# Kernel optimization log

Measured on AMD Instinct MI355X. Metric: run time of the kernel, lower is better.

Reference implementation:

```python
import jax, jax.numpy as jnp
import numpy as np

L, H = 6, 8          # depth, heads
DM, DH, M = 512, 64, 256  # d_model, d_head, nb random features
EPS = 1e-4


def sinusoidal_pe(n, d, dtype):
    pos = jnp.arange(n, dtype=jnp.float32)[:, None]
    div = jnp.exp(jnp.arange(0, d, 2, dtype=jnp.float32) * (-(np.log(10000.0) / d)))
    pe = jnp.zeros((n, d), jnp.float32)
    pe = pe.at[:, 0::2].set(jnp.sin(pos * div))
    pe = pe.at[:, 1::2].set(jnp.cos(pos * div))
    return pe.astype(dtype)


def layer_norm(x, g, b, eps=1e-5):
    mu = jnp.mean(x, -1, keepdims=True)
    var = jnp.mean(jnp.square(x - mu), -1, keepdims=True)
    return (x - mu) * jax.lax.rsqrt(var + eps) * g + b


def softmax_features(x, proj, is_query):
    # FAVOR+ positive softmax-kernel features. x: [b,h,n,dh], proj: [m,dh]
    dn = DH ** -0.25
    xd = x * dn
    u = jnp.einsum('bhnd,md->bhnm', xd, proj)            # [b,h,n,m]
    diag = 0.5 * jnp.sum(xd * xd, -1, keepdims=True)      # ||x||^2/2 (normalized)
    if is_query:
        stab = jnp.max(u, axis=-1, keepdims=True)
    else:
        stab = jnp.max(u, axis=(-2, -1), keepdims=True)
    return (M ** -0.5) * (jnp.exp(u - diag - stab) + EPS)


def split_heads(t, b, n):
    return t.reshape(b, n, H, DH).transpose(0, 2, 1, 3)   # [b,h,n,dh]


def reference(x, proj, ln1_g, ln1_b, wq, wk, wv, wo, bo, ln2_g, ln2_b, w1, b1, w2, b2):
    b, n, d = x.shape
    x = x + sinusoidal_pe(n, d, x.dtype)[None]
    for i in range(L):
        # --- FAVOR+ linear attention (pre-norm) ---
        h = layer_norm(x, ln1_g[i], ln1_b[i])
        q = split_heads(h @ wq[i], b, n)
        k = split_heads(h @ wk[i], b, n)
        v = split_heads(h @ wv[i], b, n)
        qp = softmax_features(q, proj[i], True)           # [b,h,n,m]
        kp = softmax_features(k, proj[i], False)
        ksum = jnp.sum(kp, axis=2)                         # [b,h,m]
        d_inv = 1.0 / jnp.einsum('bhnm,bhm->bhn', qp, ksum)
        ctx = jnp.einsum('bhnm,bhnd->bhmd', kp, v)         # [b,h,m,dh]
        o = jnp.einsum('bhnm,bhmd->bhnd', qp, ctx) * d_inv[..., None]
        o = o.transpose(0, 2, 1, 3).reshape(b, n, DM)
        x = x + o @ wo[i] + bo[i]
        # --- feed-forward (pre-norm, GELU) ---
        h = layer_norm(x, ln2_g[i], ln2_b[i])
        x = x + jax.nn.gelu(h @ w1[i] + b1[i], approximate=False) @ w2[i] + b2[i]
    return x


def setup_inputs() -> dict:
    key = jax.random.key(0)
    ks = jax.random.split(key, 9)
    s_in = DM ** -0.5
    s_ff = (4 * DM) ** -0.5
    return {
        'x':     jax.random.normal(ks[0], (8, 2048, DM), jnp.float32),
        'proj':  jax.random.normal(ks[1], (L, M, DH), jnp.float32),
        'ln1_g': jnp.ones((L, DM), jnp.float32),
        'ln1_b': jnp.zeros((L, DM), jnp.float32),
        'wq':    jax.random.normal(ks[2], (L, DM, DM), jnp.float32) * s_in,
        'wk':    jax.random.normal(ks[3], (L, DM, DM), jnp.float32) * s_in,
        'wv':    jax.random.normal(ks[4], (L, DM, DM), jnp.float32) * s_in,
        'wo':    jax.random.normal(ks[5], (L, DM, DM), jnp.float32) * s_in,
        'bo':    jnp.zeros((L, DM), jnp.float32),
        'ln2_g': jnp.ones((L, DM), jnp.float32),
        'ln2_b': jnp.zeros((L, DM), jnp.float32),
        'w1':    jax.random.normal(ks[6], (L, DM, 4 * DM), jnp.float32) * s_in,
        'b1':    jnp.zeros((L, 4 * DM), jnp.float32),
        'w2':    jax.random.normal(ks[7], (L, 4 * DM, DM), jnp.float32) * s_ff,
        'b2':    jnp.zeros((L, DM), jnp.float32),
    }
```

## Files before the change

kernel.cpp:

```cpp
#include <hip/hip_runtime.h>
#include <math.h>

#define LNUM 6
#define HNUM 8
#define DMODEL 512
#define DHEAD 64
#define MFEAT 256
#define BATCH 8
#define SEQ 2048
#define TOK (BATCH*SEQ)
#define BHN (BATCH*HNUM)
#define DFF 2048
#define EPSF 1e-4f
#define LN_EPS 1e-5f
#define DNRM 0.35355339059327373f
#define SMF 0.0625f

typedef unsigned short u16;
typedef __attribute__((ext_vector_type(8))) short bf16x8;
typedef __attribute__((ext_vector_type(4))) float f32x4;
#define MFMA16(a,b,c) __builtin_amdgcn_mfma_f32_16x16x32_bf16(a,b,c,0,0,0)

#define GLOAD16(g,l) __builtin_amdgcn_global_load_lds( \
    (const __attribute__((address_space(1))) void*)(g), \
    (__attribute__((address_space(3))) void*)(l), 16, 0, 0)

__device__ __forceinline__ u16 f2bf(float f){
  unsigned int u = __float_as_uint(f);
  u = (u + 0x7fffu + ((u >> 16) & 1u)) >> 16;
  return (u16)u;
}
__device__ __forceinline__ float bf2f(u16 s){
  return __uint_as_float(((unsigned int)s) << 16);
}
__device__ __forceinline__ void atomicMaxF(float* addr, float val){
  if(val >= 0.f) atomicMax((int*)addr, __float_as_int(val));
  else           atomicMin((unsigned int*)addr, __float_as_uint(val));
}
__device__ __forceinline__ float fast_gelu(float z){
  float g2 = z*(1.5957691216f + 0.07135481628f*z*z);
  return z / (1.0f + __expf(-g2));
}

__global__ void k_addpe(const float* __restrict__ x, float* __restrict__ xo){
  int idx = blockIdx.x*256 + threadIdx.x;
  int d = idx & (DMODEL-1);
  int n = (idx >> 9) & (SEQ-1);
  int j = d >> 1;
  float freq = expf((float)(2*j) * (-9.210340371976184f / (float)DMODEL));
  float ang = (float)n * freq;
  float pe = (d & 1) ? cosf(ang) : sinf(ang);
  xo[idx] = x[idx] + pe;
}

__global__ void k_ln(const float* __restrict__ x, const float* __restrict__ g,
                     const float* __restrict__ bv, u16* __restrict__ out){
  __shared__ float sred[8];
  int t = blockIdx.x, tid = threadIdx.x;
  const float2 v = ((const float2*)(x + (size_t)t*DMODEL))[tid];
  float s = v.x + v.y;
  #pragma unroll
  for(int o=32;o;o>>=1) s += __shfl_down(s,o);
  if((tid&63)==0) sred[tid>>6] = s;
  __syncthreads();
  if(tid==0) sred[4] = (sred[0]+sred[1]+sred[2]+sred[3]) * (1.0f/DMODEL);
  __syncthreads();
  float mu = sred[4];
  float dx = v.x - mu, dy = v.y - mu;
  float s2 = dx*dx + dy*dy;
  #pragma unroll
  for(int o=32;o;o>>=1) s2 += __shfl_down(s2,o);
  if((tid&63)==0) sred[tid>>6] = s2;
  __syncthreads();
  if(tid==0) sred[5] = rsqrtf((sred[0]+sred[1]+sred[2]+sred[3])*(1.0f/DMODEL) + LN_EPS);
  __syncthreads();
  float rs = sred[5];
  const float2 gg = ((const float2*)g)[tid];
  const float2 bb = ((const float2*)bv)[tid];
  ushort2 o2; o2.x = f2bf(dx*rs*gg.x + bb.x); o2.y = f2bf(dy*rs*gg.y + bb.y);
  ((ushort2*)(out + (size_t)t*DMODEL))[tid] = o2;
}

__global__ void k_pcvt(const float* __restrict__ p, u16* __restrict__ pb){
  int i = blockIdx.x*256 + threadIdx.x;
  pb[i] = f2bf(p[i]);
}

__global__ void k_wcvt_all(const float* __restrict__ wq, const float* __restrict__ wk,
                           const float* __restrict__ wv, const float* __restrict__ wo,
                           const float* __restrict__ w1, const float* __restrict__ w2,
                           u16* __restrict__ wqT, u16* __restrict__ wkT,
                           u16* __restrict__ wvT, u16* __restrict__ woT,
                           u16* __restrict__ w1T, u16* __restrict__ w2T,
                           float* __restrict__ ksum, float* __restrict__ kmax){
  int bid = blockIdx.x;
  if(bid >= 768){
    int i = (bid-768)*256 + threadIdx.x;
    ksum[i] = 0.f;
    if(i < BHN) kmax[i] = -INFINITY;
    return;
  }
  const float* src; u16* dst; int K, N, bx, by;
  if(bid < 256){
    int which = bid >> 6, sub = bid & 63;
    src = which==0 ? wq : which==1 ? wk : which==2 ? wv : wo;
    dst = which==0 ? wqT : which==1 ? wkT : which==2 ? wvT : woT;
    K = 512; N = 512; bx = sub & 7; by = sub >> 3;
  } else if(bid < 512){
    int sub = bid - 256; src = w1; dst = w1T; K = 512; N = 2048; bx = sub & 31; by = sub >> 5;
  } else {
    int sub = bid - 512; src = w2; dst = w2T; K = 2048; N = 512; bx = sub & 7; by = sub >> 3;
  }
  __shared__ float sm[64][65];
  int kt = by*64, nt = bx*64;
  int t = threadIdx.x, c = t & 63, r4 = t >> 6;
  #pragma unroll
  for(int i=0;i<16;i++){
    int kl = i*4 + r4;
    sm[kl][c] = src[(size_t)(kt+kl)*N + nt + c];
  }
  __syncthreads();
  #pragma unroll
  for(int i=0;i<16;i++){
    int nl = i*4 + r4;
    dst[(size_t)(nt+nl)*K + kt + c] = f2bf(sm[c][nl]);
  }
}

template<int EPI>
__global__ __launch_bounds__(256,4)
void k_mm(const u16* __restrict__ A, const u16* __restrict__ Bt,
          const float* __restrict__ bias, void* __restrict__ Cv,
          int Nc, int K){
  __shared__ u16 As[2][128*32];
  __shared__ u16 Bs[2][128*32];
  int tid = threadIdx.x;
  int w = tid >> 6, lane = tid & 63;
  int wr = w >> 1, wc = w & 1;
  int hi = lane >> 4, li = lane & 15;
  int row0 = blockIdx.y*128, col0 = blockIdx.x*128;
  int lr = lane >> 2;
  int cs = (lane & 3) ^ ((lane >> 3) & 3);
  const u16* gA = A  + (size_t)(row0 + w*16 + lr)*K + cs*8;
  const u16* gB = Bt + (size_t)(col0 + w*16 + lr)*K + cs*8;
  int rb = li*32 + ((hi ^ ((li>>1)&3))<<3);
  f32x4 acc[4][4] = {};

#define STAGE_MM(b,k0) { \
    GLOAD16(gA + (k0),                &As[b][(w*16)*32]);      \
    GLOAD16(gA + (size_t)64*K + (k0), &As[b][(64+w*16)*32]);   \
    GLOAD16(gB + (k0),                &Bs[b][(w*16)*32]);      \
    GLOAD16(gB + (size_t)64*K + (k0), &Bs[b][(64+w*16)*32]); }

  int nk = K >> 5;
  STAGE_MM(0, 0)
  STAGE_MM(1, 32)
  for(int t=0; t<nk; ++t){
    __builtin_amdgcn_sched_barrier(0);
    if(t+1 < nk){ asm volatile("s_waitcnt vmcnt(4)"); }
    else        { asm volatile("s_waitcnt vmcnt(0)"); }
    __builtin_amdgcn_s_barrier();
    __builtin_amdgcn_sched_barrier(0);
    const u16* pa = &As[t&1][0];
    const u16* pb = &Bs[t&1][0];
    bf16x8 bfr[4];
    #pragma unroll
    for(int q=0;q<4;q++) bfr[q] = *(const bf16x8*)&pb[rb + wc*2048 + q*512];
    #pragma unroll
    for(int i2=0;i2<4;i2++){
      bf16x8 a = *(const bf16x8*)&pa[rb + wr*2048 + i2*512];
      #pragma unroll
      for(int j2=0;j2<4;j2++)
        acc[i2][j2] = MFMA16(a, bfr[j2], acc[i2][j2]);
    }
    __builtin_amdgcn_sched_barrier(0);
    __builtin_amdgcn_s_barrier();
    __builtin_amdgcn_sched_barrier(0);
    if(t+2 < nk){ STAGE_MM(t&1, (size_t)(t+2)*32) }
  }
#undef STAGE_MM

  #pragma unroll
  for(int i2=0;i2<4;i2++){
    #pragma unroll
    for(int j2=0;j2<4;j2++){
      int col = col0 + wc*64 + j2*16 + li;
      float bcol = (EPI==2 || EPI==3) ? bias[col] : 0.f;
      if constexpr (EPI==4){
        int nb = row0 + wr*64 + i2*16 + hi*4;
        int b = nb >> 11, n = nb & (SEQ-1);
        int h = col >> 6, dh = col & 63;
        ushort4 pk;
        pk.x = f2bf(acc[i2][j2][0]); pk.y = f2bf(acc[i2][j2][1]);
        pk.z = f2bf(acc[i2][j2][2]); pk.w = f2bf(acc[i2][j2][3]);
        *(ushort4*)((u16*)Cv + (((size_t)(b*HNUM+h)*DHEAD + dh)*SEQ + n)) = pk;
      } else {
        #pragma unroll
        for(int r=0;r<4;r++){
          int row = row0 + wr*64 + i2*16 + hi*4 + r;
          float v = acc[i2][j2][r];
          if constexpr (EPI==1){
            int b = row >> 11, n = row & (SEQ-1);
            int h = col >> 6, dh = col & 63;
            ((u16*)Cv)[((size_t)(b*HNUM+h)*SEQ + n)*DHEAD + dh] = f2bf(v);
          } else if constexpr (EPI==2){
            ((float*)Cv)[(size_t)row*Nc + col] += v + bcol;
          } else {
            ((u16*)Cv)[(size_t)row*Nc + col] = f2bf(fast_gelu(v + bcol));
          }
        }
      }
    }
  }
}

__global__ __launch_bounds__(256)
void k_kmax(const u16* __restrict__ xg, const u16* __restrict__ pjb,
            float* __restrict__ kmax){
  __shared__ u16 pj[256*64];
  __shared__ u16 xs[128*64];
  __shared__ float wred[4];
  int tid = threadIdx.x, w = tid >> 6, lane = tid & 63;
  int hi = lane >> 4, li = lane & 15;
  int r0 = blockIdx.x * 128;
  int bh = r0 >> 11;
  #pragma unroll
  for(int i=0;i<8;i++){
    int idx = i*256 + tid;
    int m = idx >> 3, c = idx & 7;
    bf16x8 v = *(const bf16x8*)(pjb + m*64 + c*8);
    *(bf16x8*)&pj[m*64 + ((c ^ (m&7))<<3)] = v;
  }
  #pragma unroll
  for(int i=0;i<4;i++){
    int idx = i*256 + tid;
    int m = idx >> 3, c = idx & 7;
    bf16x8 v = *(const bf16x8*)(xg + (size_t)(r0+m)*64 + c*8);
    *(bf16x8*)&xs[m*64 + ((c ^ (m&7))<<3)] = v;
  }
  __syncthreads();
  bf16x8 bfr[2][4];
  #pragma unroll
  for(int ks=0;ks<2;ks++){
    int kc = ks*4 + hi;
    #pragma unroll
    for(int t=0;t<4;t++){
      int bc = w*64 + t*16 + li;
      bfr[ks][t] = *(const bf16x8*)&pj[bc*64 + ((kc ^ (bc&7))<<3)];
    }
  }
  float mx = -1e30f;
  #pragma unroll
  for(int i8=0;i8<8;i8++){
    f32x4 acc[4] = {};
    #pragma unroll
    for(int ks=0;ks<2;ks++){
      int kc = ks*4 + hi;
      int ar = i8*16 + li;
      bf16x8 af = *(const bf16x8*)&xs[ar*64 + ((kc ^ (ar&7))<<3)];
      #pragma unroll
      for(int j2=0;j2<4;j2++)
        acc[j2] = MFMA16(af, bfr[ks][j2], acc[j2]);
    }
    #pragma unroll
    for(int j2=0;j2<4;j2++)
      #pragma unroll
      for(int r=0;r<4;r++) mx = fmaxf(mx, acc[j2][r]);
  }
  #pragma unroll
  for(int o=32;o;o>>=1) mx = fmaxf(mx, __shfl_xor(mx,o));
  if(lane==0) wred[w] = mx;
  __syncthreads();
  if(tid==0){
    float m2 = fmaxf(fmaxf(wred[0],wred[1]), fmaxf(wred[2],wred[3]));
    atomicMaxF(&kmax[bh], m2*DNRM);
  }
}

__global__ __launch_bounds__(256)
void k_kfeat(const u16* __restrict__ xg, const u16* __restrict__ pjb,
             u16* __restrict__ outp, const float* __restrict__ kmax,
             float* __restrict__ ksum){
  __shared__ u16 pj[256*64];
  __shared__ u16 xs[128*64];
  __shared__ float dgs[128];
  int tid = threadIdx.x, w = tid >> 6, lane = tid & 63;
  int hi = lane >> 4, li = lane & 15;
  int r0 = blockIdx.x * 128;
  int bh = r0 >> 11;
  int nbase = r0 & (SEQ-1);
  #pragma unroll
  for(int i=0;i<8;i++){
    int idx = i*256 + tid;
    int m = idx >> 3, c = idx & 7;
    bf16x8 v = *(const bf16x8*)(pjb + m*64 + c*8);
    *(bf16x8*)&pj[m*64 + ((c ^ (m&7))<<3)] = v;
  }
  #pragma unroll
  for(int i=0;i<4;i++){
    int idx = i*256 + tid;
    int m = idx >> 3, c = idx & 7;
    bf16x8 v = *(const bf16x8*)(xg + (size_t)(r0+m)*64 + c*8);
    *(bf16x8*)&xs[m*64 + ((c ^ (m&7))<<3)] = v;
    float s = 0.f;
    #pragma unroll
    for(int j=0;j<8;j++){ float t = bf2f((u16)v[j]); s += t*t; }
    s += __shfl_xor(s,1); s += __shfl_xor(s,2); s += __shfl_xor(s,4);
    if((tid&7)==0) dgs[m] = 0.5f*DNRM*DNRM*s;
  }
  __syncthreads();
  bf16x8 bfr[2][4];
  #pragma unroll
  for(int ks=0;ks<2;ks++){
    int kc = ks*4 + hi;
    #pragma unroll
    for(int t=0;t<4;t++){
      int bc = w*64 + t*16 + li;
      bfr[ks][t] = *(const bf16x8*)&pj[bc*64 + ((kc ^ (bc&7))<<3)];
    }
  }
  float km = kmax[bh];
  float csum[4] = {0.f,0.f,0.f,0.f};
  #pragma unroll
  for(int i8=0;i8<8;i8++){
    f32x4 acc[4] = {};
    #pragma unroll
    for(int ks=0;ks<2;ks++){
      int kc = ks*4 + hi;
      int ar = i8*16 + li;
      bf16x8 af = *(const bf16x8*)&xs[ar*64 + ((kc ^ (ar&7))<<3)];
      #pragma unroll
      for(int j2=0;j2<4;j2++)
        acc[j2] = MFMA16(af, bfr[ks][j2], acc[j2]);
    }
    #pragma unroll
    for(int j2=0;j2<4;j2++){
      int col = w*64 + j2*16 + li;
      ushort4 pk;
      float cpart = 0.f;
      #pragma unroll
      for(int r=0;r<4;r++){
        int rl = i8*16 + hi*4 + r;
        float u = acc[j2][r]*DNRM;
        u16 eb = f2bf(SMF*(__expf(u - dgs[rl] - km) + EPSF));
        ((u16*)&pk)[r] = eb;
        cpart += bf2f(eb);
      }
      *(ushort4*)(outp + ((size_t)(bh*MFEAT + col)*SEQ + nbase + i8*16 + hi*4)) = pk;
      csum[j2] += cpart;
    }
  }
  #pragma unroll
  for(int j2=0;j2<4;j2++){
    float v = csum[j2];
    v += __shfl_xor(v,16); v += __shfl_xor(v,32);
    if(hi==0) atomicAdd(&ksum[bh*MFEAT + w*64 + j2*16 + li], v);
  }
}

__global__ __launch_bounds__(256)
void k_feato(const u16* __restrict__ xg, const u16* __restrict__ pjb,
             const u16* __restrict__ ctxt, const float* __restrict__ ksum,
             u16* __restrict__ o){
  __shared__ u16 smA[16384];
  __shared__ u16 smX[2048];
  __shared__ u16 smQ[8448];
  __shared__ float dgs[32];
  __shared__ float wred[4][32];
  __shared__ float wden[4][32];
  __shared__ float ksl[256];
  __shared__ float denl[32];
  int tid = threadIdx.x, w = tid >> 6, lane = tid & 63;
  int hi = lane >> 4, li = lane & 15;
  int r0 = blockIdx.x * 32;
  int bh = r0 >> 11;
  int b = bh >> 3, h = bh & 7;
  #pragma unroll
  for(int i=0;i<8;i++){
    int idx = i*256 + tid;
    int m = idx >> 3, c = idx & 7;
    bf16x8 v = *(const bf16x8*)(pjb + m*64 + c*8);
    *(bf16x8*)&smA[m*64 + ((c ^ (m&7))<<3)] = v;
  }
  {
    int m = tid >> 3, c = tid & 7;
    bf16x8 v = *(const bf16x8*)(xg + (size_t)(r0+m)*64 + c*8);
    *(bf16x8*)&smX[m*64 + ((c ^ (m&7))<<3)] = v;
    float s = 0.f;
    #pragma unroll
    for(int j=0;j<8;j++){ float t = bf2f((u16)v[j]); s += t*t; }
    s += __shfl_xor(s,1); s += __shfl_xor(s,2); s += __shfl_xor(s,4);
    if((tid&7)==0) dgs[m] = 0.5f*DNRM*DNRM*s;
  }
  ksl[tid] = ksum[bh*MFEAT + tid];
  __syncthreads();
  f32x4 acc[2][4] = {};
  #pragma unroll
  for(int ks=0;ks<2;ks++){
    bf16x8 af[2], bfr[4];
    int kc = ks*4 + hi;
    #pragma unroll
    for(int t=0;t<2;t++){
      int ar = t*16 + li;
      af[t] = *(const bf16x8*)&smX[ar*64 + ((kc ^ (ar&7))<<3)];
    }
    #pragma unroll
    for(int t=0;t<4;t++){
      int bc = w*64 + t*16 + li;
      bfr[t] = *(const bf16x8*)&smA[bc*64 + ((kc ^ (bc&7))<<3)];
    }
    #pragma unroll
    for(int i2=0;i2<2;i2++)
      #pragma unroll
      for(int j2=0;j2<4;j2++)
        acc[i2][j2] = MFMA16(af[i2], bfr[j2], acc[i2][j2]);
  }
  __syncthreads();
  {
    int Lc0 = w*64 + lane;
    int row0 = Lc0 >> 5, c0 = Lc0 & 31;
    const u16* gCl = ctxt + (size_t)bh*DHEAD*MFEAT + ((size_t)row0*32 + (c0 ^ (row0&7)))*8;
    #pragma unroll
    for(int i=0;i<8;i++)
      GLOAD16(gCl + i*2048, &smA[i*2048 + w*512]);
  }
  #pragma unroll
  for(int i2=0;i2<2;i2++){
    #pragma unroll
    for(int r=0;r<4;r++){
      float v = fmaxf(fmaxf(acc[i2][0][r],acc[i2][1][r]), fmaxf(acc[i2][2][r],acc[i2][3][r]));
      v = fmaxf(v, __shfl_xor(v,1)); v = fmaxf(v, __shfl_xor(v,2));
      v = fmaxf(v, __shfl_xor(v,4)); v = fmaxf(v, __shfl_xor(v,8));
      if(li==0) wred[w][i2*16 + hi*4 + r] = v;
    }
  }
  __builtin_amdgcn_sched_barrier(0);
  asm volatile("s_waitcnt lgkmcnt(0)");
  __builtin_amdgcn_s_barrier();
  __builtin_amdgcn_sched_barrier(0);
  #pragma unroll
  for(int i2=0;i2<2;i2++){
    #pragma unroll
    for(int r=0;r<4;r++){
      int rl = i2*16 + hi*4 + r;
      float rm = fmaxf(fmaxf(wred[0][rl],wred[1][rl]), fmaxf(wred[2][rl],wred[3][rl]));
      float dsum = 0.f;
      #pragma unroll
      for(int j2=0;j2<4;j2++){
        int col = w*64 + j2*16 + li;
        float u = acc[i2][j2][r]*DNRM;
        u16 eb = f2bf(SMF*(__expf(u - dgs[rl] - rm) + EPSF));
        smQ[rl*264 + col] = eb;
        dsum += bf2f(eb)*ksl[col];
      }
      dsum += __shfl_xor(dsum,1); dsum += __shfl_xor(dsum,2);
      dsum += __shfl_xor(dsum,4); dsum += __shfl_xor(dsum,8);
      if(li==0) wden[w][rl] = dsum;
    }
  }
  __builtin_amdgcn_sched_barrier(0);
  asm volatile("s_waitcnt vmcnt(0) lgkmcnt(0)");
  __builtin_amdgcn_s_barrier();
  __builtin_amdgcn_sched_barrier(0);
  if(tid < 32) denl[tid] = wden[0][tid]+wden[1][tid]+wden[2][tid]+wden[3][tid];
  f32x4 acc2[2] = {};
  #pragma unroll
  for(int s=0;s<8;s++){
    int kc = s*4 + hi;
    int bc = w*16 + li;
    bf16x8 bf = *(const bf16x8*)&smA[bc*256 + ((kc ^ (bc&7))<<3)];
    #pragma unroll
    for(int t=0;t<2;t++){
      int ar = t*16 + li;
      bf16x8 aa = *(const bf16x8*)&smQ[ar*264 + kc*8];
      acc2[t] = MFMA16(aa, bf, acc2[t]);
    }
  }
  __syncthreads();
  int nbase = r0 & (SEQ-1);
  #pragma unroll
  for(int t=0;t<2;t++){
    #pragma unroll
    for(int r=0;r<4;r++){
      int nl = t*16 + hi*4 + r;
      float di = 1.0f/denl[nl];
      o[((size_t)b*SEQ + nbase + nl)*DMODEL + h*DHEAD + w*16 + li] = f2bf(acc2[t][r]*di);
    }
  }
}

__global__ __launch_bounds__(256)
void k_ctx(const u16* __restrict__ vt, const u16* __restrict__ kpt,
           u16* __restrict__ ctxt){
  __shared__ u16 As[2][64*64];
  __shared__ u16 Bs[2][64*64];
  int tid = threadIdx.x, w = tid >> 6, lane = tid & 63;
  int wr = w >> 1, wc = w & 1;
  int hi = lane >> 4, li = lane & 15;
  int bh = blockIdx.y, mb = blockIdx.x*64;
  int lr = lane >> 3;
  int lc = (lane & 7) ^ lr;
  const u16* gA = vt  + (size_t)bh*DHEAD*SEQ + (size_t)(w*8 + lr)*SEQ + lc*8;
  const u16* gB = kpt + ((size_t)bh*MFEAT + mb + w*8 + lr)*SEQ + lc*8;
  f32x4 acc[2][2] = {};
#define STAGE_CTX(b,k0) { \
    GLOAD16(gA + (k0),                 &As[b][(w*8)*64]);      \
    GLOAD16(gA + (size_t)32*SEQ + (k0),&As[b][(32+w*8)*64]);   \
    GLOAD16(gB + (k0),                 &Bs[b][(w*8)*64]);      \
    GLOAD16(gB + (size_t)32*SEQ + (k0),&Bs[b][(32+w*8)*64]); }
  int nk = SEQ/64;
  STAGE_CTX(0, 0)
  STAGE_CTX(1, 64)
  for(int t=0; t<nk; ++t){
    __builtin_amdgcn_sched_barrier(0);
    if(t+1 < nk){ asm volatile("s_waitcnt vmcnt(4)"); }
    else        { asm volatile("s_waitcnt vmcnt(0)"); }
    __builtin_amdgcn_s_barrier();
    __builtin_amdgcn_sched_barrier(0);
    const u16* pa = &As[t&1][0];
    const u16* pb = &Bs[t&1][0];
    #pragma unroll
    for(int ks=0;ks<2;ks++){
      bf16x8 af[2], bfr[2];
      int kc = ks*4 + hi;
      #pragma unroll
      for(int q=0;q<2;q++){
        int ar = wr*32 + q*16 + li;
        af[q] = *(const bf16x8*)&pa[ar*64 + ((kc ^ (ar&7))<<3)];
        int bc = wc*32 + q*16 + li;
        bfr[q] = *(const bf16x8*)&pb[bc*64 + ((kc ^ (bc&7))<<3)];
      }
      #pragma unroll
      for(int i2=0;i2<2;i2++)
        #pragma unroll
        for(int j2=0;j2<2;j2++)
          acc[i2][j2] = MFMA16(af[i2], bfr[j2], acc[i2][j2]);
    }
    __builtin_amdgcn_sched_barrier(0);
    __builtin_amdgcn_s_barrier();
    __builtin_amdgcn_sched_barrier(0);
    if(t+2 < nk){ STAGE_CTX(t&1, (size_t)(t+2)*64) }
  }
#undef STAGE_CTX
  #pragma unroll
  for(int i2=0;i2<2;i2++)
    #pragma unroll
    for(int j2=0;j2<2;j2++){
      int m = mb + wc*32 + j2*16 + li;
      #pragma unroll
      for(int r=0;r<4;r++){
        int dh = wr*32 + i2*16 + hi*4 + r;
        ctxt[((size_t)bh*DHEAD + dh)*MFEAT + m] = f2bf(acc[i2][j2][r]);
      }
    }
}

extern "C" void kernel_launch(void* const* d_in, const int* in_sizes, int n_in,
                              void* d_out, int out_size, void* d_ws, size_t ws_size,
                              hipStream_t stream){
  (void)in_sizes; (void)n_in; (void)out_size; (void)ws_size;
  const float* x    = (const float*)d_in[0];
  const float* proj = (const float*)d_in[1];
  const float* ln1g = (const float*)d_in[2];
  const float* ln1b = (const float*)d_in[3];
  const float* wq   = (const float*)d_in[4];
  const float* wk   = (const float*)d_in[5];
  const float* wv   = (const float*)d_in[6];
  const float* wo   = (const float*)d_in[7];
  const float* bo   = (const float*)d_in[8];
  const float* ln2g = (const float*)d_in[9];
  const float* ln2b = (const float*)d_in[10];
  const float* w1   = (const float*)d_in[11];
  const float* b1   = (const float*)d_in[12];
  const float* w2   = (const float*)d_in[13];
  const float* b2   = (const float*)d_in[14];
  float* xo = (float*)d_out;

  char* ws = (char*)d_ws;
  u16* bufH  = (u16*)ws;  ws += (size_t)TOK*DMODEL*2;
  u16* bufA  = (u16*)ws;  ws += (size_t)TOK*DMODEL*2;
  u16* featb = (u16*)ws;  ws += (size_t)BHN*SEQ*MFEAT*2;
  u16* ctxt  = (u16*)ws;  ws += (size_t)BHN*DHEAD*MFEAT*2;
  u16* wT    = (u16*)ws;  ws += (size_t)3*1048576*2;
  u16* pjb   = (u16*)ws;  ws += (size_t)LNUM*MFEAT*DHEAD*2;
  float* ksum= (float*)ws; ws += (size_t)BHN*MFEAT*4;
  float* kmax= (float*)ws; ws += 256;

  u16* wqT = wT;
  u16* wkT = wT +  262144;
  u16* wvT = wT +  524288;
  u16* woT = wT +  786432;
  u16* w1T = wT + 1048576;
  u16* w2T = wT + 2097152;

  k_addpe<<<(TOK*DMODEL)/256, 256, 0, stream>>>(x, xo);
  k_pcvt<<<(LNUM*MFEAT*DHEAD)/256, 256, 0, stream>>>(proj, pjb);

  for(int l=0; l<LNUM; l++){
    const u16* pj_l = pjb + (size_t)l*MFEAT*DHEAD;
    k_wcvt_all<<<832, 256, 0, stream>>>(wq + (size_t)l*262144, wk + (size_t)l*262144,
                                        wv + (size_t)l*262144, wo + (size_t)l*262144,
                                        w1 + (size_t)l*1048576, w2 + (size_t)l*1048576,
                                        wqT, wkT, wvT, woT, w1T, w2T, ksum, kmax);
    k_ln<<<TOK, 256, 0, stream>>>(xo, ln1g + l*DMODEL, ln1b + l*DMODEL, bufH);
    k_mm<1><<<dim3(4,128), 256, 0, stream>>>(bufH, wkT, nullptr, bufA, DMODEL, DMODEL);
    k_kmax<<<(BHN*SEQ)/128, 256, 0, stream>>>(bufA, pj_l, kmax);
    k_kfeat<<<(BHN*SEQ)/128, 256, 0, stream>>>(bufA, pj_l, featb, kmax, ksum);
    k_mm<4><<<dim3(4,128), 256, 0, stream>>>(bufH, wvT, nullptr, bufA, DMODEL, DMODEL);
    k_ctx<<<dim3(4,BHN), 256, 0, stream>>>(bufA, featb, ctxt);
    k_mm<1><<<dim3(4,128), 256, 0, stream>>>(bufH, wqT, nullptr, bufA, DMODEL, DMODEL);
    k_feato<<<(BHN*SEQ)/32, 256, 0, stream>>>(bufA, pj_l, ctxt, ksum, bufH);
    k_mm<2><<<dim3(4,128), 256, 0, stream>>>(bufH, woT, bo + l*DMODEL, xo, DMODEL, DMODEL);
    k_ln<<<TOK, 256, 0, stream>>>(xo, ln2g + l*DMODEL, ln2b + l*DMODEL, bufA);
    k_mm<3><<<dim3(16,128), 256, 0, stream>>>(bufA, w1T, b1 + l*DFF, featb, DFF, DMODEL);
    k_mm<2><<<dim3(4,128), 256, 0, stream>>>(featb, w2T, b2 + l*DMODEL, xo, DMODEL, DFF);
  }
}
```

Measured before the change: 2.181 ms.

## Process 64 query rows per block in k_feato with 512 threads

Doubles the rows handled by each k_feato block from 32 to 64 and the threads from 256 to 512, splitting the 8 waves into two row groups. The projection matrix and the context tile loaded into shared memory are now reused across twice as many rows, halving that per-row load traffic and the number of blocks. In exchange, each block uses more LDS and has a larger barrier domain, which may lower occupancy.

```diff
diff --git a/kernel.cpp b/kernel.cpp
--- a/kernel.cpp
+++ b/kernel.cpp
@@ -358,26 +358,27 @@
   }
 }
 
-__global__ __launch_bounds__(256)
+__global__ __launch_bounds__(512)
 void k_feato(const u16* __restrict__ xg, const u16* __restrict__ pjb,
              const u16* __restrict__ ctxt, const float* __restrict__ ksum,
              u16* __restrict__ o){
   __shared__ u16 smA[16384];
-  __shared__ u16 smX[2048];
-  __shared__ u16 smQ[8448];
-  __shared__ float dgs[32];
-  __shared__ float wred[4][32];
-  __shared__ float wden[4][32];
+  __shared__ u16 smX[4096];
+  __shared__ u16 smQ[64*264];
+  __shared__ float dgs[64];
+  __shared__ float wred[2][4][32];
+  __shared__ float wden[2][4][32];
   __shared__ float ksl[256];
-  __shared__ float denl[32];
+  __shared__ float denl[64];
   int tid = threadIdx.x, w = tid >> 6, lane = tid & 63;
   int hi = lane >> 4, li = lane & 15;
-  int r0 = blockIdx.x * 32;
+  int g = w >> 2, wq = w & 3;
+  int r0 = blockIdx.x * 64;
   int bh = r0 >> 11;
   int b = bh >> 3, h = bh & 7;
   #pragma unroll
-  for(int i=0;i<8;i++){
-    int idx = i*256 + tid;
+  for(int i=0;i<4;i++){
+    int idx = i*512 + tid;
     int m = idx >> 3, c = idx & 7;
     bf16x8 v = *(const bf16x8*)(pjb + m*64 + c*8);
     *(bf16x8*)&smA[m*64 + ((c ^ (m&7))<<3)] = v;
@@ -392,7 +393,7 @@
     s += __shfl_xor(s,1); s += __shfl_xor(s,2); s += __shfl_xor(s,4);
     if((tid&7)==0) dgs[m] = 0.5f*DNRM*DNRM*s;
   }
-  ksl[tid] = ksum[bh*MFEAT + tid];
+  if(tid < 256) ksl[tid] = ksum[bh*MFEAT + tid];
   __syncthreads();
   f32x4 acc[2][4] = {};
   #pragma unroll
@@ -401,12 +402,12 @@
     int kc = ks*4 + hi;
     #pragma unroll
     for(int t=0;t<2;t++){
-      int ar = t*16 + li;
+      int ar = g*32 + t*16 + li;
       af[t] = *(const bf16x8*)&smX[ar*64 + ((kc ^ (ar&7))<<3)];
     }
     #pragma unroll
     for(int t=0;t<4;t++){
-      int bc = w*64 + t*16 + li;
+      int bc = wq*64 + t*16 + li;
       bfr[t] = *(const bf16x8*)&smA[bc*64 + ((kc ^ (bc&7))<<3)];
     }
     #pragma unroll
@@ -417,12 +418,11 @@
   }
   __syncthreads();
   {
-    int Lc0 = w*64 + lane;
-    int row0 = Lc0 >> 5, c0 = Lc0 & 31;
-    const u16* gCl = ctxt + (size_t)bh*DHEAD*MFEAT + ((size_t)row0*32 + (c0 ^ (row0&7)))*8;
-    #pragma unroll
-    for(int i=0;i<8;i++)
-      GLOAD16(gCl + i*2048, &smA[i*2048 + w*512]);
+    int gch = (tid & 31) ^ ((tid >> 5) & 7);
+    const u16* gCl = ctxt + (size_t)bh*DHEAD*MFEAT + (size_t)(tid>>5)*MFEAT + gch*8;
+    #pragma unroll
+    for(int i=0;i<4;i++)
+      GLOAD16(gCl + (size_t)i*16*MFEAT, &smA[i*4096 + w*512]);
   }
   #pragma unroll
   for(int i2=0;i2<2;i2++){
@@ -431,7 +431,7 @@
       float v = fmaxf(fmaxf(acc[i2][0][r],acc[i2][1][r]), fmaxf(acc[i2][2][r],acc[i2][3][r]));
       v = fmaxf(v, __shfl_xor(v,1)); v = fmaxf(v, __shfl_xor(v,2));
       v = fmaxf(v, __shfl_xor(v,4)); v = fmaxf(v, __shfl_xor(v,8));
-      if(li==0) wred[w][i2*16 + hi*4 + r] = v;
+      if(li==0) wred[g][wq][i2*16 + hi*4 + r] = v;
     }
   }
   __builtin_amdgcn_sched_barrier(0);
@@ -443,35 +443,41 @@
     #pragma unroll
     for(int r=0;r<4;r++){
       int rl = i2*16 + hi*4 + r;
-      float rm = fmaxf(fmaxf(wred[0][rl],wred[1][rl]), fmaxf(wred[2][rl],wred[3][rl]));
+      int row = g*32 + rl;
+      float rm = fmaxf(fmaxf(wred[g][0][rl],wred[g][1][rl]),
+                       fmaxf(wred[g][2][rl],wred[g][3][rl]));
       float dsum = 0.f;
       #pragma unroll
       for(int j2=0;j2<4;j2++){
-        int col = w*64 + j2*16 + li;
+        int col = wq*64 + j2*16 + li;
         float u = acc[i2][j2][r]*DNRM;
-        u16 eb = f2bf(SMF*(__expf(u - dgs[rl] - rm) + EPSF));
-        smQ[rl*264 + col] = eb;
+        u16 eb = f2bf(SMF*(__expf(u - dgs[row] - rm) + EPSF));
+        smQ[row*264 + col] = eb;
         dsum += bf2f(eb)*ksl[col];
       }
       dsum += __shfl_xor(dsum,1); dsum += __shfl_xor(dsum,2);
       dsum += __shfl_xor(dsum,4); dsum += __shfl_xor(dsum,8);
-      if(li==0) wden[w][rl] = dsum;
+      if(li==0) wden[g][wq][rl] = dsum;
     }
   }
   __builtin_amdgcn_sched_barrier(0);
   asm volatile("s_waitcnt vmcnt(0) lgkmcnt(0)");
   __builtin_amdgcn_s_barrier();
   __builtin_amdgcn_sched_barrier(0);
-  if(tid < 32) denl[tid] = wden[0][tid]+wden[1][tid]+wden[2][tid]+wden[3][tid];
+  if(tid < 64){
+    int gg = tid >> 5, rr = tid & 31;
+    denl[tid] = wden[gg][0][rr]+wden[gg][1][rr]+wden[gg][2][rr]+wden[gg][3][rr];
+  }
+  int d4 = w >> 1, g2 = w & 1;
   f32x4 acc2[2] = {};
   #pragma unroll
   for(int s=0;s<8;s++){
     int kc = s*4 + hi;
-    int bc = w*16 + li;
+    int bc = d4*16 + li;
     bf16x8 bf = *(const bf16x8*)&smA[bc*256 + ((kc ^ (bc&7))<<3)];
     #pragma unroll
     for(int t=0;t<2;t++){
-      int ar = t*16 + li;
+      int ar = g2*32 + t*16 + li;
       bf16x8 aa = *(const bf16x8*)&smQ[ar*264 + kc*8];
       acc2[t] = MFMA16(aa, bf, acc2[t]);
     }
@@ -482,9 +488,9 @@
   for(int t=0;t<2;t++){
     #pragma unroll
     for(int r=0;r<4;r++){
-      int nl = t*16 + hi*4 + r;
+      int nl = g2*32 + t*16 + hi*4 + r;
       float di = 1.0f/denl[nl];
-      o[((size_t)b*SEQ + nbase + nl)*DMODEL + h*DHEAD + w*16 + li] = f2bf(acc2[t][r]*di);
+      o[((size_t)b*SEQ + nbase + nl)*DMODEL + h*DHEAD + d4*16 + li] = f2bf(acc2[t][r]*di);
     }
   }
 }
@@ -609,7 +615,7 @@
     k_mm<4><<<dim3(4,128), 256, 0, stream>>>(bufH, wvT, nullptr, bufA, DMODEL, DMODEL);
     k_ctx<<<dim3(4,BHN), 256, 0, stream>>>(bufA, featb, ctxt);
     k_mm<1><<<dim3(4,128), 256, 0, stream>>>(bufH, wqT, nullptr, bufA, DMODEL, DMODEL);
-    k_feato<<<(BHN*SEQ)/32, 256, 0, stream>>>(bufA, pj_l, ctxt, ksum, bufH);
+    k_feato<<<(BHN*SEQ)/64, 512, 0, stream>>>(bufA, pj_l, ctxt, ksum, bufH);
     k_mm<2><<<dim3(4,128), 256, 0, stream>>>(bufH, woT, bo + l*DMODEL, xo, DMODEL, DMODEL);
     k_ln<<<TOK, 256, 0, stream>>>(xo, ln2g + l*DMODEL, ln2b + l*DMODEL, bufA);
     k_mm<3><<<dim3(16,128), 256, 0, stream>>>(bufA, w1T, b1 + l*DFF, featb, DFF, DMODEL);
```

Result: faster. 2.079 ms (-4.7%).
